# Performance work log

Hardware: AMD Instinct MI355X
Metric: run time of the kernel (lower is better)

## Reference

```python
import jax, jax.numpy as jnp
import numpy as np

WINDOW = 7
N_HEADS = 4
EMBED = 128
N_TOK = WINDOW * WINDOW  # 49
N_WIN = 64               # windows per image (56x56 feature map / 7)
BATCH_IMG = 64
B = N_WIN * BATCH_IMG    # 4096


def make_rel_index(w):
    ch = np.arange(w)
    coords = np.stack(np.meshgrid(ch, ch), axis=0).reshape(2, -1)  # (2, w*w)
    rel = coords[:, :, None] - coords[:, None, :]                  # (2, N, N)
    rel = rel.transpose(1, 2, 0)
    rel[:, :, 0] += w - 1
    rel[:, :, 1] += w - 1
    rel[:, :, 0] *= 2 * w - 1
    return jnp.asarray(rel.sum(-1), dtype=jnp.int32)               # (N, N)


def setup_inputs() -> dict:
    key = jax.random.key(0)
    ks = jax.random.split(key, 6)
    x = jax.random.normal(ks[0], (B, N_TOK, EMBED), dtype=jnp.float32)
    qkv_w = jax.random.normal(ks[1], (EMBED, 3 * EMBED), dtype=jnp.float32) * (EMBED ** -0.5)
    qkv_b = jnp.zeros((3 * EMBED,), dtype=jnp.float32)
    proj_w = jax.random.normal(ks[2], (EMBED, EMBED), dtype=jnp.float32) * (EMBED ** -0.5)
    proj_b = jnp.zeros((EMBED,), dtype=jnp.float32)
    bias_table = jax.random.normal(ks[3], ((2 * WINDOW - 1) ** 2, N_HEADS), dtype=jnp.float32) * 0.02
    # shift mask: additive, 0 or large negative; use random binary * -100 to mimic Swin shift mask
    mask_bits = jax.random.bernoulli(ks[4], 0.2, (N_WIN, N_TOK, N_TOK))
    mask = jnp.where(mask_bits, jnp.float32(-100.0), jnp.float32(0.0))
    rel_index = make_rel_index(WINDOW)
    return {"x": x, "qkv_w": qkv_w, "qkv_b": qkv_b, "proj_w": proj_w,
            "proj_b": proj_b, "bias_table": bias_table, "mask": mask,
            "rel_index": rel_index}


def reference(x, qkv_w, qkv_b, proj_w, proj_b, bias_table, mask, rel_index):
    Bt, N, C = x.shape
    h = N_HEADS
    d = C // h
    scale = d ** -0.5
    qkv = (x @ qkv_w + qkv_b).reshape(Bt, N, 3, h, d)
    q, k, v = jnp.moveaxis(qkv, 2, 0)                      # each (B, N, h, d)
    q = q * scale
    attn = jnp.einsum('bnhd,bmhd->bhnm', q, k)             # (B, h, N, N)
    bias = bias_table[rel_index.reshape(-1)].reshape(N, N, h)
    attn = attn + jnp.transpose(bias, (2, 0, 1))[None]     # add rel-pos bias
    nW = mask.shape[0]
    attn = attn.reshape(Bt // nW, nW, h, N, N) + mask[None, :, None]
    attn = jax.nn.softmax(attn.reshape(Bt, h, N, N), axis=-1)
    out = jnp.einsum('bhnm,bmhd->bnhd', attn, v).reshape(Bt, N, C)
    return out @ proj_w + proj_b
```

## Files before the change

kernel.cpp:

```cpp
#include <hip/hip_runtime.h>

#define NTOK 49
#define CDIM 128
#define NH 4
#define NWIN 64

typedef unsigned short u16;
typedef unsigned int u32;
typedef __bf16 bf16x8 __attribute__((ext_vector_type(8)));
typedef float f32x4 __attribute__((ext_vector_type(4)));
typedef u16 u16x4 __attribute__((ext_vector_type(4)));

union Frag { u32 u[4]; bf16x8 v; };

__device__ __forceinline__ u16 f2bf(float f) {
  union { __bf16 h; u16 u; } c;
  c.h = (__bf16)f;
  return c.u;
}
__device__ __forceinline__ u32 pack2(float a, float b) {
  return (u32)f2bf(a) | ((u32)f2bf(b) << 16);
}
__device__ __forceinline__ bf16x8 ld8(const u16* p) { return *(const bf16x8*)p; }

__device__ __forceinline__ void build_frag(u32 u[4], u32 x0, u32 y0, u32 x1, u32 y1,
                                           int quad, int ln) {
#pragma unroll
  for (int p = 0; p < 4; ++p) {
    int src = ((2 * (quad & 1) + (p >> 1)) << 4) | ln;
    int a0 = __shfl((int)((p & 1) ? y0 : x0), src);
    int a1 = __shfl((int)((p & 1) ? y1 : x1), src);
    u[p] = (u32)((quad < 2) ? a0 : a1);
  }
}

__global__ void prep_kernel(const float* __restrict__ qkv_w,
                            const float* __restrict__ proj_w,
                            const float* __restrict__ bias_table,
                            const float* __restrict__ mask,
                            const int* __restrict__ rel_index,
                            u16* __restrict__ wqkvT,
                            u16* __restrict__ wprojT,
                            float* __restrict__ cmb) {
  int i = blockIdx.x * 256 + threadIdx.x;
  if (i < 384 * 128) {
    int n = i >> 7, k = i & 127;
    wqkvT[i] = f2bf(qkv_w[k * 384 + n]);
  }
  if (i < 128 * 128) {
    int n = i >> 7, k = i & 127;
    wprojT[i] = f2bf(proj_w[k * 128 + n]);
  }
  int m = i & 63, q = (i >> 6) & 63, hh = (i >> 12) & 3, win = i >> 14;
  float v = -1e30f;
  if (q < NTOK && m < NTOK)
    v = bias_table[rel_index[q * NTOK + m] * NH + hh] + mask[(win * NTOK + q) * NTOK + m];
  cmb[i] = v;
}

#define RGN(h) (8192 + (h) * 4608)

__device__ __forceinline__ int xsw(int row, int col) {
  return (row << 7) + ((((col >> 3) ^ (row & 15)) << 3) | (col & 7));
}

__global__ __launch_bounds__(256, 2)
void swin_fused(const float* __restrict__ x, const float* __restrict__ qkv_b,
                const float* __restrict__ proj_b, const u16* __restrict__ wqkvT,
                const u16* __restrict__ wprojT, const float* __restrict__ cmb,
                float* __restrict__ out) {
  __shared__ u16 lds[26624];
  const int tid  = threadIdx.x;
  const int w    = tid >> 6;
  const int lane = tid & 63;
  const int ln   = lane & 15;
  const int quad = lane >> 4;
  const int b    = blockIdx.x;
  const int win  = b & (NWIN - 1);
  const float scale = 0.17677669529663687f;

  {
    const float4* x4 = (const float4*)(x + (size_t)b * (NTOK * CDIM));
    for (int i = tid; i < (NTOK * CDIM) / 4; i += 256) {
      float4 f = x4[i];
      int e = i << 2;
      int row = e >> 7, col = e & 127;
      u16x4 v;
      v[0] = f2bf(f.x); v[1] = f2bf(f.y); v[2] = f2bf(f.z); v[3] = f2bf(f.w);
      *(u16x4*)&lds[xsw(row, col)] = v;
    }
    for (int i = tid; i < (15 * CDIM) / 4; i += 256) {
      int e = i << 2;
      int row = NTOK + (e >> 7), col = e & 127;
      u16x4 v = {0, 0, 0, 0};
      *(u16x4*)&lds[xsw(row, col)] = v;
    }
  }
  __syncthreads();

  u32 vbx[4][2], vby[4][2];
  {
    bf16x8 af[4][4];
#pragma unroll
    for (int tm = 0; tm < 4; ++tm)
#pragma unroll
      for (int ks = 0; ks < 4; ++ks)
        af[tm][ks] = ld8(&lds[xsw(tm * 16 + ln, ks * 32 + quad * 8)]);

#pragma unroll
    for (int tl = 0; tl < 6; ++tl) {
      int sect = tl >> 1, tc = tl & 1;
      int colg = sect * 128 + w * 32 + tc * 16 + ln;
      bf16x8 bw[4];
#pragma unroll
      for (int ks = 0; ks < 4; ++ks)
        bw[ks] = ld8(wqkvT + colg * 128 + ks * 32 + quad * 8);
      float cb = qkv_b[colg];
#pragma unroll
      for (int tm = 0; tm < 4; ++tm) {
        f32x4 acc = {0.f, 0.f, 0.f, 0.f};
#pragma unroll
        for (int ks = 0; ks < 4; ++ks)
          acc = __builtin_amdgcn_mfma_f32_16x16x32_bf16(af[tm][ks], bw[ks], acc, 0, 0, 0);
        int row0 = tm * 16 + quad * 4;
        if (sect == 0) {
#pragma unroll
          for (int r = 0; r < 4; ++r)
            lds[RGN(w) + (row0 + r) * 36 + tc * 16 + ln] = f2bf((acc[r] + cb) * scale);
        } else if (sect == 1) {
#pragma unroll
          for (int r = 0; r < 4; ++r)
            lds[RGN(w) + 2304 + (row0 + r) * 36 + tc * 16 + ln] = f2bf(acc[r] + cb);
        } else {
          vbx[tm][tc] = pack2(acc[0] + cb, acc[1] + cb);
          vby[tm][tc] = pack2(acc[2] + cb, acc[3] + cb);
        }
      }
    }
  }

  {
    bf16x8 aq[4], bk[4];
#pragma unroll
    for (int t = 0; t < 4; ++t) {
      aq[t] = ld8(&lds[RGN(w) + (t * 16 + ln) * 36 + quad * 8]);
      bk[t] = ld8(&lds[RGN(w) + 2304 + (t * 16 + ln) * 36 + quad * 8]);
    }
    f32x4 s[4][4];
#pragma unroll
    for (int tn = 0; tn < 4; ++tn)
#pragma unroll
      for (int tm = 0; tm < 4; ++tm) {
        f32x4 z = {0.f, 0.f, 0.f, 0.f};
        s[tm][tn] = __builtin_amdgcn_mfma_f32_16x16x32_bf16(bk[tn], aq[tm], z, 0, 0, 0);
      }

    Frag bv[2][2];
#pragma unroll
    for (int ks = 0; ks < 2; ++ks)
#pragma unroll
      for (int tc = 0; tc < 2; ++tc)
        build_frag(bv[ks][tc].u, vbx[2 * ks][tc], vby[2 * ks][tc],
                   vbx[2 * ks + 1][tc], vby[2 * ks + 1][tc], quad, ln);

    const float* cbp = cmb + ((size_t)((win << 2) | w) << 12);
#pragma unroll
    for (int tm = 0; tm < 4; ++tm) {
      float e[4][4];
      float tsum = 0.f;
#pragma unroll
      for (int tn = 0; tn < 4; ++tn) {
        f32x4 c4 = *(const f32x4*)&cbp[(tm * 16 + ln) * 64 + tn * 16 + quad * 4];
#pragma unroll
        for (int r = 0; r < 4; ++r)
          e[tn][r] = __expf(s[tm][tn][r] + c4[r]);
        tsum += (e[tn][0] + e[tn][1]) + (e[tn][2] + e[tn][3]);
      }
      tsum += __shfl_xor(tsum, 16);
      tsum += __shfl_xor(tsum, 32);
      float iv = 1.0f / fmaxf(tsum, 1e-30f);

      u32 px[4], py[4];
#pragma unroll
      for (int tn = 0; tn < 4; ++tn) {
        px[tn] = pack2(e[tn][0] * iv, e[tn][1] * iv);
        py[tn] = pack2(e[tn][2] * iv, e[tn][3] * iv);
      }

      f32x4 o[2];
#pragma unroll
      for (int tc = 0; tc < 2; ++tc) { f32x4 z = {0.f,0.f,0.f,0.f}; o[tc] = z; }
#pragma unroll
      for (int ks = 0; ks < 2; ++ks) {
        Frag pa;
        build_frag(pa.u, px[2 * ks], py[2 * ks], px[2 * ks + 1], py[2 * ks + 1], quad, ln);
#pragma unroll
        for (int tc = 0; tc < 2; ++tc)
          o[tc] = __builtin_amdgcn_mfma_f32_16x16x32_bf16(pa.v, bv[ks][tc].v, o[tc], 0, 0, 0);
      }

      int row0 = tm * 16 + quad * 4;
#pragma unroll
      for (int tc = 0; tc < 2; ++tc)
#pragma unroll
        for (int r = 0; r < 4; ++r)
          lds[RGN(w) + (row0 + r) * 36 + tc * 16 + ln] = f2bf(o[tc][r]);
    }
  }
  __syncthreads();

  {
    bf16x8 aof[4][4];
#pragma unroll
    for (int tm = 0; tm < 4; ++tm)
#pragma unroll
      for (int ks = 0; ks < 4; ++ks)
        aof[tm][ks] = ld8(&lds[RGN(ks) + (tm * 16 + ln) * 36 + quad * 8]);
#pragma unroll
    for (int tj = 0; tj < 2; ++tj) {
      int colg = w * 32 + tj * 16 + ln;
      bf16x8 bw[4];
#pragma unroll
      for (int ks = 0; ks < 4; ++ks)
        bw[ks] = ld8(wprojT + colg * 128 + ks * 32 + quad * 8);
      float pb = proj_b[colg];
#pragma unroll
      for (int tm = 0; tm < 4; ++tm) {
        f32x4 acc = {0.f, 0.f, 0.f, 0.f};
#pragma unroll
        for (int ks = 0; ks < 4; ++ks)
          acc = __builtin_amdgcn_mfma_f32_16x16x32_bf16(aof[tm][ks], bw[ks], acc, 0, 0, 0);
        int row0 = tm * 16 + quad * 4;
#pragma unroll
        for (int r = 0; r < 4; ++r) {
          int rr = row0 + r;
          if (rr < NTOK)
            out[((size_t)b * NTOK + rr) * CDIM + colg] = acc[r] + pb;
        }
      }
    }
  }
}

extern "C" void kernel_launch(void* const* d_in, const int* in_sizes, int n_in,
                              void* d_out, int out_size, void* d_ws, size_t ws_size,
                              hipStream_t stream) {
  const float* x          = (const float*)d_in[0];
  const float* qkv_w      = (const float*)d_in[1];
  const float* qkv_b      = (const float*)d_in[2];
  const float* proj_w     = (const float*)d_in[3];
  const float* proj_b     = (const float*)d_in[4];
  const float* bias_table = (const float*)d_in[5];
  const float* mask       = (const float*)d_in[6];
  const int*   rel_index  = (const int*)d_in[7];

  u16*   wqkvT  = (u16*)d_ws;
  u16*   wprojT = wqkvT + 384 * 128;
  float* cmb    = (float*)((char*)d_ws + 131072);

  const int Bt = in_sizes[0] / (NTOK * CDIM);

  prep_kernel<<<4096, 256, 0, stream>>>(qkv_w, proj_w, bias_table, mask, rel_index,
                                        wqkvT, wprojT, cmb);
  swin_fused<<<Bt, 256, 0, stream>>>(x, qkv_b, proj_b, wqkvT, wprojT, cmb, (float*)d_out);
}
```

Measured before the change: 289.3 us.

## Keep Q and K in registers via shuffles instead of staging through LDS

Q and K projections are now computed with swapped MFMA operands so their outputs land in registers in a transposed layout. They are then rearranged into MFMA input fragments with cross-lane shuffles rather than written to and reloaded from shared memory. The QKV loop is reordered to run per row tile, and the score MFMAs are computed per tile inside the softmax loop. This shrinks the LDS allocation from about 52KB to about 34KB and removes the LDS round trip, but it adds shuffle instructions and register pressure from holding Q, K and V fragments at once.

```diff
diff --git a/kernel.cpp b/kernel.cpp
--- a/kernel.cpp
+++ b/kernel.cpp
@@ -58,7 +58,7 @@
   cmb[i] = v;
 }
 
-#define RGN(h) (8192 + (h) * 4608)
+#define AOFF 8192
 
 __device__ __forceinline__ int xsw(int row, int col) {
   return (row << 7) + ((((col >> 3) ^ (row & 15)) << 3) | (col & 7));
@@ -69,7 +69,7 @@
                 const float* __restrict__ proj_b, const u16* __restrict__ wqkvT,
                 const u16* __restrict__ wprojT, const float* __restrict__ cmb,
                 float* __restrict__ out) {
-  __shared__ u16 lds[26624];
+  __shared__ u16 lds[17408];
   const int tid  = threadIdx.x;
   const int w    = tid >> 6;
   const int lane = tid & 63;
@@ -98,63 +98,57 @@
   }
   __syncthreads();
 
-  u32 vbx[4][2], vby[4][2];
-  {
-    bf16x8 af[4][4];
-#pragma unroll
-    for (int tm = 0; tm < 4; ++tm)
+  u32 qx[4][2], qy[4][2], kx[4][2], ky[4][2], vbx[4][2], vby[4][2];
+  {
+#pragma unroll
+    for (int tm = 0; tm < 4; ++tm) {
+      bf16x8 af[4];
 #pragma unroll
       for (int ks = 0; ks < 4; ++ks)
-        af[tm][ks] = ld8(&lds[xsw(tm * 16 + ln, ks * 32 + quad * 8)]);
-
-#pragma unroll
-    for (int tl = 0; tl < 6; ++tl) {
-      int sect = tl >> 1, tc = tl & 1;
-      int colg = sect * 128 + w * 32 + tc * 16 + ln;
-      bf16x8 bw[4];
-#pragma unroll
-      for (int ks = 0; ks < 4; ++ks)
-        bw[ks] = ld8(wqkvT + colg * 128 + ks * 32 + quad * 8);
-      float cb = qkv_b[colg];
-#pragma unroll
-      for (int tm = 0; tm < 4; ++tm) {
+        af[ks] = ld8(&lds[xsw(tm * 16 + ln, ks * 32 + quad * 8)]);
+
+#pragma unroll
+      for (int sect = 0; sect < 2; ++sect) {
+#pragma unroll
+        for (int tc = 0; tc < 2; ++tc) {
+          int colb = sect * 128 + w * 32 + tc * 16;
+          bf16x8 bw[4];
+#pragma unroll
+          for (int ks = 0; ks < 4; ++ks)
+            bw[ks] = ld8(wqkvT + (colb + ln) * 128 + ks * 32 + quad * 8);
+          f32x4 cb4 = *(const f32x4*)&qkv_b[colb + quad * 4];
+          f32x4 acc = {0.f, 0.f, 0.f, 0.f};
+#pragma unroll
+          for (int ks = 0; ks < 4; ++ks)
+            acc = __builtin_amdgcn_mfma_f32_16x16x32_bf16(bw[ks], af[ks], acc, 0, 0, 0);
+          if (sect == 0) {
+            qx[tm][tc] = pack2((acc[0] + cb4[0]) * scale, (acc[1] + cb4[1]) * scale);
+            qy[tm][tc] = pack2((acc[2] + cb4[2]) * scale, (acc[3] + cb4[3]) * scale);
+          } else {
+            kx[tm][tc] = pack2(acc[0] + cb4[0], acc[1] + cb4[1]);
+            ky[tm][tc] = pack2(acc[2] + cb4[2], acc[3] + cb4[3]);
+          }
+        }
+      }
+#pragma unroll
+      for (int tc = 0; tc < 2; ++tc) {
+        int colg = 256 + w * 32 + tc * 16 + ln;
+        bf16x8 bw[4];
+#pragma unroll
+        for (int ks = 0; ks < 4; ++ks)
+          bw[ks] = ld8(wqkvT + colg * 128 + ks * 32 + quad * 8);
+        float cb = qkv_b[colg];
         f32x4 acc = {0.f, 0.f, 0.f, 0.f};
 #pragma unroll
         for (int ks = 0; ks < 4; ++ks)
-          acc = __builtin_amdgcn_mfma_f32_16x16x32_bf16(af[tm][ks], bw[ks], acc, 0, 0, 0);
-        int row0 = tm * 16 + quad * 4;
-        if (sect == 0) {
-#pragma unroll
-          for (int r = 0; r < 4; ++r)
-            lds[RGN(w) + (row0 + r) * 36 + tc * 16 + ln] = f2bf((acc[r] + cb) * scale);
-        } else if (sect == 1) {
-#pragma unroll
-          for (int r = 0; r < 4; ++r)
-            lds[RGN(w) + 2304 + (row0 + r) * 36 + tc * 16 + ln] = f2bf(acc[r] + cb);
-        } else {
-          vbx[tm][tc] = pack2(acc[0] + cb, acc[1] + cb);
-          vby[tm][tc] = pack2(acc[2] + cb, acc[3] + cb);
-        }
-      }
-    }
-  }
-
-  {
-    bf16x8 aq[4], bk[4];
-#pragma unroll
-    for (int t = 0; t < 4; ++t) {
-      aq[t] = ld8(&lds[RGN(w) + (t * 16 + ln) * 36 + quad * 8]);
-      bk[t] = ld8(&lds[RGN(w) + 2304 + (t * 16 + ln) * 36 + quad * 8]);
-    }
-    f32x4 s[4][4];
-#pragma unroll
-    for (int tn = 0; tn < 4; ++tn)
-#pragma unroll
-      for (int tm = 0; tm < 4; ++tm) {
-        f32x4 z = {0.f, 0.f, 0.f, 0.f};
-        s[tm][tn] = __builtin_amdgcn_mfma_f32_16x16x32_bf16(bk[tn], aq[tm], z, 0, 0, 0);
-      }
-
+          acc = __builtin_amdgcn_mfma_f32_16x16x32_bf16(af[ks], bw[ks], acc, 0, 0, 0);
+        vbx[tm][tc] = pack2(acc[0] + cb, acc[1] + cb);
+        vby[tm][tc] = pack2(acc[2] + cb, acc[3] + cb);
+      }
+    }
+  }
+
+  {
     Frag bv[2][2];
 #pragma unroll
     for (int ks = 0; ks < 2; ++ks)
@@ -162,10 +156,23 @@
       for (int tc = 0; tc < 2; ++tc)
         build_frag(bv[ks][tc].u, vbx[2 * ks][tc], vby[2 * ks][tc],
                    vbx[2 * ks + 1][tc], vby[2 * ks + 1][tc], quad, ln);
+    Frag kf[4];
+#pragma unroll
+    for (int tn = 0; tn < 4; ++tn)
+      build_frag(kf[tn].u, kx[tn][0], ky[tn][0], kx[tn][1], ky[tn][1], quad, ln);
 
     const float* cbp = cmb + ((size_t)((win << 2) | w) << 12);
 #pragma unroll
     for (int tm = 0; tm < 4; ++tm) {
+      Frag qf;
+      build_frag(qf.u, qx[tm][0], qy[tm][0], qx[tm][1], qy[tm][1], quad, ln);
+      f32x4 s[4];
+#pragma unroll
+      for (int tn = 0; tn < 4; ++tn) {
+        f32x4 z = {0.f, 0.f, 0.f, 0.f};
+        s[tn] = __builtin_amdgcn_mfma_f32_16x16x32_bf16(kf[tn].v, qf.v, z, 0, 0, 0);
+      }
+
       float e[4][4];
       float tsum = 0.f;
 #pragma unroll
@@ -173,7 +180,7 @@
         f32x4 c4 = *(const f32x4*)&cbp[(tm * 16 + ln) * 64 + tn * 16 + quad * 4];
 #pragma unroll
         for (int r = 0; r < 4; ++r)
-          e[tn][r] = __expf(s[tm][tn][r] + c4[r]);
+          e[tn][r] = __expf(s[tn][r] + c4[r]);
         tsum += (e[tn][0] + e[tn][1]) + (e[tn][2] + e[tn][3]);
       }
       tsum += __shfl_xor(tsum, 16);
@@ -204,7 +211,7 @@
       for (int tc = 0; tc < 2; ++tc)
 #pragma unroll
         for (int r = 0; r < 4; ++r)
-          lds[RGN(w) + (row0 + r) * 36 + tc * 16 + ln] = f2bf(o[tc][r]);
+          lds[AOFF + w * 2304 + (row0 + r) * 36 + tc * 16 + ln] = f2bf(o[tc][r]);
     }
   }
   __syncthreads();
@@ -215,7 +222,7 @@
     for (int tm = 0; tm < 4; ++tm)
 #pragma unroll
       for (int ks = 0; ks < 4; ++ks)
-        aof[tm][ks] = ld8(&lds[RGN(ks) + (tm * 16 + ln) * 36 + quad * 8]);
+        aof[tm][ks] = ld8(&lds[AOFF + ks * 2304 + (tm * 16 + ln) * 36 + quad * 8]);
 #pragma unroll
     for (int tj = 0; tj < 2; ++tj) {
       int colg = w * 32 + tj * 16 + ln;
```

After: 306.9 us. 6.1% more time.
